# Performance work log

Measured on AMD Instinct MI355X. Metric: run time of the kernel, lower is better.

## Reference

```python
import jax, jax.numpy as jnp
import numpy as np

N, S, E, H = 4, 4096, 1024, 16
D = E // H  # 64


def setup_inputs() -> dict:
    key = jax.random.key(0)
    ks = jax.random.split(key, 6)
    scale = 0.02
    x = jax.random.normal(ks[0], (N, S, E), dtype=jnp.float32)
    Wq = jax.random.normal(ks[1], (E, E), dtype=jnp.float32) * scale
    Wk = jax.random.normal(ks[2], (E, E), dtype=jnp.float32) * scale
    Wv = jax.random.normal(ks[3], (E, E), dtype=jnp.float32) * scale
    Wo = jax.random.normal(ks[4], (E, E), dtype=jnp.float32) * scale
    bo = jax.random.normal(ks[5], (E,), dtype=jnp.float32) * scale
    return {"x": x, "Wq": Wq, "Wk": Wk, "Wv": Wv, "Wo": Wo, "bo": bo}


def reference(x, Wq, Wk, Wv, Wo, bo):
    n, s, _ = x.shape
    # torch nn.Linear(bias=False): y = x @ W.T  (W stored as [out, in])
    q = (x @ Wq.T).reshape(n, s, H, D).transpose(0, 2, 1, 3)  # (N, H, S, D)
    k = (x @ Wk.T).reshape(n, s, H, D).transpose(0, 2, 1, 3)  # (N, H, S, D)
    v = (x @ Wv.T).reshape(n, s, H, D).transpose(0, 2, 1, 3)  # (N, H, S, D)
    # Faithful to source: einsum subscripts applied to the PERMUTED (N,H,S,D)
    # tensors, so label q->H, h->S. energy: (N, H, H, S)
    energy = jnp.einsum('nqhd,nkhd->nqkh', q, k)
    attention = jax.nn.softmax(energy / (D ** 0.5), axis=3)
    # 'nqkh,nvhd->nqhd': k and v are independently summed free indices
    out = jnp.einsum('nqkh,nvhd->nqhd', attention, v).reshape(n, s, E)  # (N,S,E)
    return out @ Wo.T + bo
```

## Files before the change

### kernel.cpp

```cpp
#include <hip/hip_runtime.h>
#include <stdint.h>

typedef unsigned short u16;
typedef unsigned int   u32;
typedef __attribute__((ext_vector_type(8))) short short8;
typedef __attribute__((ext_vector_type(4))) float f32x4;
typedef __attribute__((ext_vector_type(8))) u16   u16x8;
typedef __attribute__((ext_vector_type(4))) u16   u16x4;

static constexpr size_t NX = (size_t)4 * 4096 * 1024;
static constexpr size_t NW = (size_t)1024 * 1024;

static constexpr size_t OFF_XB   = 0;
static constexpr size_t OFF_EN   = 0;
static constexpr size_t OFF_QK   = 33554432;
static constexpr size_t OFF_WQB  = 100663296;
static constexpr size_t OFF_WKB  = 102760448;
static constexpr size_t OFF_WOB  = 104857600;
static constexpr size_t OFF_WVST = 106954752;
static constexpr size_t OFF_VS   = 107216896;
static constexpr size_t OFF_GMAX = 111411200;
static constexpr size_t OFF_INVZ = 111415296;
static constexpr size_t OFF_ST   = 111419392;

static __device__ __forceinline__ u16 f2bf(float f) {
    u32 u = __builtin_bit_cast(u32, f);
    u += 0x7fffu + ((u >> 16) & 1u);
    return (u16)(u >> 16);
}
static __device__ __forceinline__ float bf2f(u16 v) {
    u32 u = ((u32)v) << 16;
    return __builtin_bit_cast(float, u);
}

#if __has_builtin(__builtin_amdgcn_global_load_lds)
#define HAVE_GLOAD_LDS 1
static __device__ __forceinline__ void gload_lds16(const void* g, void* l) {
    __builtin_amdgcn_global_load_lds(
        (__attribute__((address_space(1))) void*)(uintptr_t)g,
        (__attribute__((address_space(3))) void*)(uintptr_t)l,
        16, 0, 0);
}
#endif

#if __has_builtin(__builtin_amdgcn_sched_barrier)
#define SCHED_FENCE() __builtin_amdgcn_sched_barrier(0)
#else
#define SCHED_FENCE()
#endif

__global__ __launch_bounds__(256)
void cvt_all_kernel(const float* __restrict__ x, const float* __restrict__ wq,
                    const float* __restrict__ wk, const float* __restrict__ wv,
                    const float* __restrict__ wo,
                    u16* __restrict__ xb, u16* __restrict__ wqb,
                    u16* __restrict__ wkb, u16* __restrict__ wob,
                    u16* __restrict__ Bvs)
{
    const int blk = blockIdx.x;
    if (blk < 9728) {
        size_t i = ((size_t)blk * 256 + threadIdx.x) * 8;
        const float* s; u16* dst; size_t o;
        if (i < NX) { s = x; dst = xb; o = i; }
        else {
            size_t r = i - NX;
            int w = (int)(r >> 20);
            o = r & (NW - 1);
            s   = (w == 0) ? wq  : (w == 1) ? wk  : wo;
            dst = (w == 0) ? wqb : (w == 1) ? wkb : wob;
        }
        f32x4 a = *(const f32x4*)&s[o];
        f32x4 c = *(const f32x4*)&s[o + 4];
        u16x8 v;
        v[0]=f2bf(a[0]); v[1]=f2bf(a[1]); v[2]=f2bf(a[2]); v[3]=f2bf(a[3]);
        v[4]=f2bf(c[0]); v[5]=f2bf(c[1]); v[6]=f2bf(c[2]); v[7]=f2bf(c[3]);
        *(u16x8*)&dst[o] = v;
    } else {
        int idx = (blk - 9728) * 256 + threadIdx.x;
        int d = idx >> 10;
        int e = idx & 1023;
        float s = 0.f;
        #pragma unroll
        for (int h = 0; h < 16; ++h) s += wv[(size_t)(h * 64 + d) * 1024 + e];
        Bvs[(size_t)d * 1024 + e] = f2bf(s);
    }
}

__global__ __launch_bounds__(512, 2)
void gemm_qk(const u16* __restrict__ A, const u16* __restrict__ Bw,
             u16* __restrict__ C, int M, int N, int K, int lognbx)
{
    __shared__ u16 lds[65536];
    const int tid  = threadIdx.x;
    const int wave = tid >> 6;
    const int lane = tid & 63;

    const int nwg = gridDim.x;
    const int swz = ((int)blockIdx.x & 7) * (nwg >> 3) + ((int)blockIdx.x >> 3);
    const long col0 = (long)(swz & ((1 << lognbx) - 1)) * 256;
    const long row0 = (long)(swz >> lognbx) * 256;

    const int wr2 = wave >> 2;
    const int wc2 = wave & 3;
    const int fr  = lane & 15;
    const int kq  = lane >> 4;
    const int rxor = fr & 7;

    const int t255  = tid & 255;
    const int halfA = tid >> 8;
    const int gAsrc = (t255 & 7) ^ ((t255 >> 3) & 7);
    const u16* sA = A + (size_t)(row0 + halfA * 128 + (t255 >> 3)) * K + gAsrc * 8;
    const int dA = halfA * 8192 + t255 * 8;

    const int u  = (tid & 127) | ((tid >> 1) & 128);
    const int bh = (tid >> 7) & 1;
    const int gBsrc = (u & 7) ^ ((u >> 3) & 7);
    const u16* sB = Bw + (size_t)(col0 + bh * 128 + (u >> 3)) * K + gBsrc * 8;
    const int dB = bh * 8192 + u * 8;

    auto STAGE = [&](int buf, int k0) {
        #pragma unroll
        for (int l = 0; l < 4; ++l) {
#ifdef HAVE_GLOAD_LDS
            gload_lds16(sA + (size_t)l * 32 * K + k0, &lds[buf * 16384 + dA + l * 2048]);
            gload_lds16(sB + (size_t)l * 32 * K + k0, &lds[32768 + buf * 16384 + dB + l * 2048]);
#else
            *(short8*)&lds[buf * 16384 + dA + l * 2048] =
                *(const short8*)(sA + (size_t)l * 32 * K + k0);
            *(short8*)&lds[32768 + buf * 16384 + dB + l * 2048] =
                *(const short8*)(sB + (size_t)l * 32 * K + k0);
#endif
        }
    };

    f32x4 acc[8][4] = {};

    STAGE(0, 0);
    __syncthreads();

    const int nt = K >> 6;
    for (int t = 0; t < nt; ++t) {
        const int cur = t & 1;
        const int base  = cur * 16384;
        const int bbase = 32768 + cur * 16384;

        if (t + 1 < nt) STAGE(cur ^ 1, (t + 1) << 6);

        short8 af[4][2], ag[4][2], bf[2][2], bg[2][2];
        #pragma unroll
        for (int m = 0; m < 4; ++m) {
            const int row = wr2 * 128 + m * 16 + fr;
            #pragma unroll
            for (int kk = 0; kk < 2; ++kk)
                af[m][kk] = *(const short8*)&lds[base + row * 64 + (((kk << 2) | kq) ^ rxor) * 8];
        }
        #pragma unroll
        for (int n = 0; n < 2; ++n) {
            const int col = wc2 * 64 + n * 16 + fr;
            #pragma unroll
            for (int kk = 0; kk < 2; ++kk)
                bf[n][kk] = *(const short8*)&lds[bbase + col * 64 + (((kk << 2) | kq) ^ rxor) * 8];
        }
        #pragma unroll
        for (int m = 0; m < 4; ++m) {
            const int row = wr2 * 128 + 64 + m * 16 + fr;
            #pragma unroll
            for (int kk = 0; kk < 2; ++kk)
                ag[m][kk] = *(const short8*)&lds[base + row * 64 + (((kk << 2) | kq) ^ rxor) * 8];
        }
        SCHED_FENCE();

        __builtin_amdgcn_s_setprio(1);
        #pragma unroll
        for (int kk = 0; kk < 2; ++kk)
            #pragma unroll
            for (int m = 0; m < 4; ++m)
                #pragma unroll
                for (int n = 0; n < 2; ++n)
                    acc[m][n] = __builtin_amdgcn_mfma_f32_16x16x32_bf16(af[m][kk], bf[n][kk], acc[m][n], 0, 0, 0);
        __builtin_amdgcn_s_setprio(0);

        #pragma unroll
        for (int n = 0; n < 2; ++n) {
            const int col = wc2 * 64 + (n + 2) * 16 + fr;
            #pragma unroll
            for (int kk = 0; kk < 2; ++kk)
                bg[n][kk] = *(const short8*)&lds[bbase + col * 64 + (((kk << 2) | kq) ^ rxor) * 8];
        }
        SCHED_FENCE();

        __builtin_amdgcn_s_setprio(1);
        #pragma unroll
        for (int kk = 0; kk < 2; ++kk)
            #pragma unroll
            for (int m = 0; m < 4; ++m)
                #pragma unroll
                for (int n = 0; n < 2; ++n)
                    acc[m + 4][n] = __builtin_amdgcn_mfma_f32_16x16x32_bf16(ag[m][kk], bf[n][kk], acc[m + 4][n], 0, 0, 0);
        #pragma unroll
        for (int kk = 0; kk < 2; ++kk)
            #pragma unroll
            for (int m = 0; m < 4; ++m)
                #pragma unroll
                for (int n = 0; n < 2; ++n)
                    acc[m][n + 2] = __builtin_amdgcn_mfma_f32_16x16x32_bf16(af[m][kk], bg[n][kk], acc[m][n + 2], 0, 0, 0);
        #pragma unroll
        for (int kk = 0; kk < 2; ++kk)
            #pragma unroll
            for (int m = 0; m < 4; ++m)
                #pragma unroll
                for (int n = 0; n < 2; ++n)
                    acc[m + 4][n + 2] = __builtin_amdgcn_mfma_f32_16x16x32_bf16(ag[m][kk], bg[n][kk], acc[m + 4][n + 2], 0, 0, 0);
        __builtin_amdgcn_s_setprio(0);

        __syncthreads();
    }

    #pragma unroll
    for (int m = 0; m < 8; ++m) {
        #pragma unroll
        for (int n = 0; n < 4; ++n) {
            long gr = row0 + wr2 * 128 + m * 16 + kq * 4;
            long gc = col0 + wc2 * 64 + n * 16 + fr;
            #pragma unroll
            for (int j = 0; j < 4; ++j)
                C[(gr + j) * N + gc] = f2bf(acc[m][n][j]);
        }
    }
}

__global__ __launch_bounds__(256)
void gemm_vs(const u16* __restrict__ A, const u16* __restrict__ Bw,
             u16* __restrict__ C)
{
    __shared__ u16 lsA[2][64 * 32];
    __shared__ u16 lsB[2][64 * 32];
    const int tid  = threadIdx.x;
    const int wave = tid >> 6;
    const int lane = tid & 63;
    const long row0 = (long)blockIdx.x * 64;
    const int wr = (wave >> 1) * 32;
    const int wc = (wave & 1) * 32;
    const int fr = lane & 15;
    const int k8 = (lane >> 4) * 8;

    f32x4 acc[2][2] = {};
    const int c0 = tid;
    const u16* pa = &A [(row0 + (c0 >> 2)) * 1024 + (c0 & 3) * 8];
    const u16* pb = &Bw[((size_t)(c0 >> 2)) * 1024 + (c0 & 3) * 8];

    auto STAGE = [&](int buf, int k0) {
#ifdef HAVE_GLOAD_LDS
        gload_lds16(pa + k0, &lsA[buf][wave * 512]);
        gload_lds16(pb + k0, &lsB[buf][wave * 512]);
#else
        *(short8*)&lsA[buf][(size_t)c0 * 8] = *(const short8*)(pa + k0);
        *(short8*)&lsB[buf][(size_t)c0 * 8] = *(const short8*)(pb + k0);
#endif
    };

    STAGE(0, 0);
    __syncthreads();
    for (int t = 0; t < 32; ++t) {
        const int cur = t & 1;
        if (t + 1 < 32) STAGE(cur ^ 1, (t + 1) << 5);
        short8 af[2], bf[2];
        #pragma unroll
        for (int m = 0; m < 2; ++m)
            af[m] = *(const short8*)&lsA[cur][(wr + m * 16 + fr) * 32 + k8];
        #pragma unroll
        for (int n = 0; n < 2; ++n)
            bf[n] = *(const short8*)&lsB[cur][(wc + n * 16 + fr) * 32 + k8];
        #pragma unroll
        for (int m = 0; m < 2; ++m)
            #pragma unroll
            for (int n = 0; n < 2; ++n)
                acc[m][n] = __builtin_amdgcn_mfma_f32_16x16x32_bf16(af[m], bf[n], acc[m][n], 0, 0, 0);
        __syncthreads();
    }

    const int orow = (lane >> 4) * 4;
    #pragma unroll
    for (int m = 0; m < 2; ++m) {
        #pragma unroll
        for (int n = 0; n < 2; ++n) {
            long gr = row0 + wr + m * 16 + orow;
            int  gc = wc + n * 16 + fr;
            #pragma unroll
            for (int j = 0; j < 4; ++j)
                C[(gr + j) * 64 + gc] = f2bf(acc[m][n][j]);
        }
    }
}

__global__ __launch_bounds__(256)
void energy_stats_kernel(const u16* __restrict__ QKb, float* __restrict__ E,
                         float* __restrict__ pmax, float* __restrict__ psum)
{
    __shared__ float red[4][64][8];
    const int wave = threadIdx.x >> 6, lane = threadIdx.x & 63;
    const size_t s0 = (size_t)blockIdx.x * 64 + wave * 16;
    const int hh = lane & 15;
    const int kg = lane >> 4;
    float m[4] = {-3.4e38f, -3.4e38f, -3.4e38f, -3.4e38f};
    float z[4] = {0.f, 0.f, 0.f, 0.f};

    for (int s = 0; s < 16; ++s) {
        const u16* qrow = QKb + (s0 + s) * 2048;
        short8 a0 = *(const short8*)&qrow[hh * 64 + kg * 8];
        short8 a1 = *(const short8*)&qrow[hh * 64 + 32 + kg * 8];
        short8 b0 = *(const short8*)&qrow[1024 + hh * 64 + kg * 8];
        short8 b1 = *(const short8*)&qrow[1024 + hh * 64 + 32 + kg * 8];
        f32x4 acc = {};
        acc = __builtin_amdgcn_mfma_f32_16x16x32_bf16(a0, b0, acc, 0, 0, 0);
        acc = __builtin_amdgcn_mfma_f32_16x16x32_bf16(a1, b1, acc, 0, 0, 0);
        float* o = E + (s0 + s) * 256;
        #pragma unroll
        for (int r = 0; r < 4; ++r) {
            const float v = acc[r];
            o[(kg * 4 + r) * 16 + hh] = v;
            const float mn = fmaxf(m[r], v);
            z[r] = z[r] * __expf((m[r] - mn) * 0.125f) + __expf((v - mn) * 0.125f);
            m[r] = mn;
        }
    }
    #pragma unroll
    for (int r = 0; r < 4; ++r) { red[wave][lane][r] = m[r]; red[wave][lane][4 + r] = z[r]; }
    __syncthreads();

    const int t = threadIdx.x;
    const int i = t >> 4, j = t & 15;
    const int ln = (i >> 2) * 16 + j, r = i & 3;
    float M = -3.4e38f, Z = 0.f;
    #pragma unroll
    for (int w = 0; w < 4; ++w) {
        const float mw = red[w][ln][r], zw = red[w][ln][4 + r];
        const float mn = fmaxf(M, mw);
        Z = Z * __expf((M - mn) * 0.125f) + zw * __expf((mw - mn) * 0.125f);
        M = mn;
    }
    pmax[blockIdx.x * 256 + t] = M;
    psum[blockIdx.x * 256 + t] = Z;
}

__global__ __launch_bounds__(256)
void stats_comb(const float* __restrict__ pmax, const float* __restrict__ psum,
                float* __restrict__ gmax, float* __restrict__ invZ)
{
    const int n = blockIdx.x, p = threadIdx.x;
    float m = -3.4e38f;
    for (int c = 0; c < 64; ++c) m = fmaxf(m, pmax[(n * 64 + c) * 256 + p]);
    float z = 0.f;
    for (int c = 0; c < 64; ++c)
        z += psum[(n * 64 + c) * 256 + p] * __expf((pmax[(n * 64 + c) * 256 + p] - m) * 0.125f);
    gmax[n * 256 + p] = m;
    invZ[n * 256 + p] = 1.0f / z;
}

__global__ __launch_bounds__(256)
void g_kernel(const u16* __restrict__ Vsb, const u16* __restrict__ Wob,
              u16* __restrict__ G)
{
    __shared__ u16 lA[64 * 64];
    __shared__ u16 lB[256 * 64];
    const int tid = threadIdx.x;
    const int wave = tid >> 6, lane = tid & 63;
    const int op = blockIdx.x, uc = blockIdx.y, sl = blockIdx.z;

    {
        const int j = tid >> 2;
        const size_t srow = (size_t)16 * (64 * uc + j) + sl;
        #pragma unroll
        for (int h = 0; h < 2; ++h) {
            const int g = (tid & 3) + h * 4;
            u16x8 v = *(const u16x8*)&Vsb[srow * 64 + g * 8];
            *(u16x8*)&lA[j * 64 + ((g ^ (j & 7)) * 8)] = v;
        }
    }
    {
        const size_t o = (size_t)op * 256 + tid;
        #pragma unroll
        for (int g = 0; g < 8; ++g) {
            u16x8 v = *(const u16x8*)&Wob[o * 1024 + 64 * sl + g * 8];
            *(u16x8*)&lB[tid * 64 + ((g ^ (tid & 7)) * 8)] = v;
        }
    }
    __syncthreads();

    const int fr = lane & 15, kq = lane >> 4;
    f32x4 acc[4][4] = {};
    #pragma unroll
    for (int kk = 0; kk < 2; ++kk) {
        short8 af[4], bq[4];
        #pragma unroll
        for (int m = 0; m < 4; ++m) {
            const int j = m * 16 + fr;
            af[m] = *(const short8*)&lA[j * 64 + (((kq + 4 * kk) ^ (j & 7)) * 8)];
        }
        #pragma unroll
        for (int n = 0; n < 4; ++n) {
            const int o = wave * 64 + n * 16 + fr;
            bq[n] = *(const short8*)&lB[o * 64 + (((kq + 4 * kk) ^ (o & 7)) * 8)];
        }
        #pragma unroll
        for (int m = 0; m < 4; ++m)
            #pragma unroll
            for (int n = 0; n < 4; ++n)
                acc[m][n] = __builtin_amdgcn_mfma_f32_16x16x32_bf16(af[m], bq[n], acc[m][n], 0, 0, 0);
    }

    #pragma unroll
    for (int m = 0; m < 4; ++m) {
        #pragma unroll
        for (int n = 0; n < 4; ++n) {
            const int ocol = op * 256 + wave * 64 + n * 16 + fr;
            #pragma unroll
            for (int jj = 0; jj < 4; ++jj) {
                const int j = m * 16 + kq * 4 + jj;
                G[((size_t)16 * (64 * uc + j) + sl) * 1024 + ocol] = f2bf(acc[m][n][jj]);
            }
        }
    }
}

__global__ __launch_bounds__(256)
void comb_kernel(const float* __restrict__ En, const float* __restrict__ gmax,
                 const float* __restrict__ invZ, const u16* __restrict__ G,
                 const float* __restrict__ bo, float* __restrict__ out)
{
    __shared__ float sm[256], sz[256], sa[256];
    const int b = blockIdx.x;
    const int n = b >> 8, c = b & 255;
    const int t = threadIdx.x;
    sm[t] = gmax[n * 256 + t];
    sz[t] = invZ[n * 256 + t];
    __syncthreads();
    {
        const int sl = t >> 4, i = t & 15;
        const float* e = En + ((size_t)n * 4096 + c * 16 + sl) * 256 + i * 16;
        float a = 0.f;
        #pragma unroll
        for (int j = 0; j < 16; ++j)
            a += __expf((e[j] - sm[i * 16 + j]) * 0.125f) * sz[i * 16 + j];
        sa[sl * 16 + i] = a;
    }
    __syncthreads();

    const int o0 = t * 4;
    const u16* gp = G + ((size_t)n * 4096 + c * 16) * 1024 + o0;
    f32x4 g[16];
    #pragma unroll
    for (int sl = 0; sl < 16; ++sl) {
        u16x4 gv = *(const u16x4*)&gp[(size_t)sl * 1024];
        g[sl][0] = bf2f(gv[0]); g[sl][1] = bf2f(gv[1]);
        g[sl][2] = bf2f(gv[2]); g[sl][3] = bf2f(gv[3]);
    }
    const f32x4 b4 = *(const f32x4*)&bo[o0];
    #pragma unroll
    for (int i = 0; i < 16; ++i) {
        f32x4 acc = b4;
        #pragma unroll
        for (int sl = 0; sl < 16; ++sl) {
            const float a = sa[sl * 16 + i];
            acc[0] += a * g[sl][0];
            acc[1] += a * g[sl][1];
            acc[2] += a * g[sl][2];
            acc[3] += a * g[sl][3];
        }
        *(f32x4*)&out[((size_t)n * 4096 + i * 256 + c) * 1024 + o0] = acc;
    }
}

extern "C" void kernel_launch(void* const* d_in, const int* in_sizes, int n_in,
                              void* d_out, int out_size, void* d_ws, size_t ws_size,
                              hipStream_t stream)
{
    const float* x  = (const float*)d_in[0];
    const float* Wq = (const float*)d_in[1];
    const float* Wk = (const float*)d_in[2];
    const float* Wv = (const float*)d_in[3];
    const float* Wo = (const float*)d_in[4];
    const float* bo = (const float*)d_in[5];
    float* out = (float*)d_out;
    char* ws = (char*)d_ws;

    u16*   xb   = (u16*)  (ws + OFF_XB);
    float* En   = (float*)(ws + OFF_EN);
    u16*   QKb  = (u16*)  (ws + OFF_QK);
    u16*   G    = (u16*)  (ws + OFF_QK);
    u16*   Wqb  = (u16*)  (ws + OFF_WQB);
    u16*   Wkb  = (u16*)  (ws + OFF_WKB);
    u16*   Wob  = (u16*)  (ws + OFF_WOB);
    u16*   Bvs  = (u16*)  (ws + OFF_WVST);
    u16*   Vsb  = (u16*)  (ws + OFF_VS);
    float* gmax = (float*)(ws + OFF_GMAX);
    float* invZ = (float*)(ws + OFF_INVZ);
    float* pmax = (float*)(ws + OFF_ST);
    float* psum = (float*)(ws + OFF_ST + 262144);

    cvt_all_kernel<<<9984, 256, 0, stream>>>(x, Wq, Wk, Wv, Wo, xb, Wqb, Wkb, Wob, Bvs);

    gemm_qk<<<512, 512, 0, stream>>>(xb, Wqb, QKb, 16384, 2048, 1024, 3);
    gemm_vs<<<256, 256, 0, stream>>>(xb, Bvs, Vsb);

    energy_stats_kernel<<<256, 256, 0, stream>>>(QKb, En, pmax, psum);
    stats_comb<<<4, 256, 0, stream>>>(pmax, psum, gmax, invZ);

    g_kernel<<<dim3(4, 16, 16), 256, 0, stream>>>(Vsb, Wob, G);

    comb_kernel<<<1024, 256, 0, stream>>>(En, gmax, invZ, G, bo, out);
}
```

Baseline: 171.9 us.

## Widen gemm_vs to 512 threads with swizzled LDS and double energy-stats grid

gemm_vs now runs 8 waves per block. Half the threads stage A and half stage B, each wave computes a 16x32 tile, and LDS columns are XOR-swizzled to reduce bank conflicts. energy_stats_kernel processes 8 rows per wave over 512 blocks instead of 16 rows over 256, which doubles the partial stats buffer. stats_comb is unrolled with four independent accumulators over 128 partials. The aim is more parallelism and latency hiding on these small kernels, at the cost of more partial-reduction work and more blocks to schedule.

```diff
diff --git a/kernel.cpp b/kernel.cpp
--- a/kernel.cpp
+++ b/kernel.cpp
@@ -12,7 +12,6 @@
 static constexpr size_t NW = (size_t)1024 * 1024;
 
 static constexpr size_t OFF_XB   = 0;
-static constexpr size_t OFF_EN   = 0;
 static constexpr size_t OFF_QK   = 33554432;
 static constexpr size_t OFF_WQB  = 100663296;
 static constexpr size_t OFF_WKB  = 102760448;
@@ -229,7 +228,7 @@
     }
 }
 
-__global__ __launch_bounds__(256)
+__global__ __launch_bounds__(512)
 void gemm_vs(const u16* __restrict__ A, const u16* __restrict__ Bw,
              u16* __restrict__ C)
 {
@@ -239,23 +238,27 @@
     const int wave = tid >> 6;
     const int lane = tid & 63;
     const long row0 = (long)blockIdx.x * 64;
-    const int wr = (wave >> 1) * 32;
+    const int wr = (wave >> 1) * 16;
     const int wc = (wave & 1) * 32;
     const int fr = lane & 15;
-    const int k8 = (lane >> 4) * 8;
-
-    f32x4 acc[2][2] = {};
-    const int c0 = tid;
-    const u16* pa = &A [(row0 + (c0 >> 2)) * 1024 + (c0 & 3) * 8];
-    const u16* pb = &Bw[((size_t)(c0 >> 2)) * 1024 + (c0 & 3) * 8];
+    const int kq = lane >> 4;
+    const int rx = (fr >> 1) & 3;
+
+    f32x4 acc[2] = {};
+    const int g = tid & 255;
+    const int grow = g >> 2;
+    const int gsw  = (g & 3) ^ ((grow >> 1) & 3);
+    const bool isA = tid < 256;
+    const u16* src = isA ? &A [(row0 + grow) * 1024 + gsw * 8]
+                         : &Bw[((size_t)grow) * 1024 + gsw * 8];
 
     auto STAGE = [&](int buf, int k0) {
 #ifdef HAVE_GLOAD_LDS
-        gload_lds16(pa + k0, &lsA[buf][wave * 512]);
-        gload_lds16(pb + k0, &lsB[buf][wave * 512]);
+        if (isA) gload_lds16(src + k0, &lsA[buf][wave * 512]);
+        else     gload_lds16(src + k0, &lsB[buf][(wave - 4) * 512]);
 #else
-        *(short8*)&lsA[buf][(size_t)c0 * 8] = *(const short8*)(pa + k0);
-        *(short8*)&lsB[buf][(size_t)c0 * 8] = *(const short8*)(pb + k0);
+        if (isA) *(short8*)&lsA[buf][(size_t)g * 8] = *(const short8*)(src + k0);
+        else     *(short8*)&lsB[buf][(size_t)g * 8] = *(const short8*)(src + k0);
 #endif
     };
 
@@ -264,32 +267,23 @@
     for (int t = 0; t < 32; ++t) {
         const int cur = t & 1;
         if (t + 1 < 32) STAGE(cur ^ 1, (t + 1) << 5);
-        short8 af[2], bf[2];
-        #pragma unroll
-        for (int m = 0; m < 2; ++m)
-            af[m] = *(const short8*)&lsA[cur][(wr + m * 16 + fr) * 32 + k8];
+        short8 af, bf[2];
+        af = *(const short8*)&lsA[cur][(wr + fr) * 32 + ((kq ^ rx) * 8)];
         #pragma unroll
         for (int n = 0; n < 2; ++n)
-            bf[n] = *(const short8*)&lsB[cur][(wc + n * 16 + fr) * 32 + k8];
-        #pragma unroll
-        for (int m = 0; m < 2; ++m)
-            #pragma unroll
-            for (int n = 0; n < 2; ++n)
-                acc[m][n] = __builtin_amdgcn_mfma_f32_16x16x32_bf16(af[m], bf[n], acc[m][n], 0, 0, 0);
+            bf[n] = *(const short8*)&lsB[cur][(wc + n * 16 + fr) * 32 + ((kq ^ rx) * 8)];
+        #pragma unroll
+        for (int n = 0; n < 2; ++n)
+            acc[n] = __builtin_amdgcn_mfma_f32_16x16x32_bf16(af, bf[n], acc[n], 0, 0, 0);
         __syncthreads();
     }
 
-    const int orow = (lane >> 4) * 4;
-    #pragma unroll
-    for (int m = 0; m < 2; ++m) {
-        #pragma unroll
-        for (int n = 0; n < 2; ++n) {
-            long gr = row0 + wr + m * 16 + orow;
-            int  gc = wc + n * 16 + fr;
-            #pragma unroll
-            for (int j = 0; j < 4; ++j)
-                C[(gr + j) * 64 + gc] = f2bf(acc[m][n][j]);
-        }
+    const int orow = kq * 4;
+    #pragma unroll
+    for (int n = 0; n < 2; ++n) {
+        #pragma unroll
+        for (int j = 0; j < 4; ++j)
+            C[(row0 + wr + orow + j) * 64 + wc + n * 16 + fr] = f2bf(acc[n][j]);
     }
 }
 
@@ -299,13 +293,13 @@
 {
     __shared__ float red[4][64][8];
     const int wave = threadIdx.x >> 6, lane = threadIdx.x & 63;
-    const size_t s0 = (size_t)blockIdx.x * 64 + wave * 16;
+    const size_t s0 = (size_t)blockIdx.x * 32 + wave * 8;
     const int hh = lane & 15;
     const int kg = lane >> 4;
     float m[4] = {-3.4e38f, -3.4e38f, -3.4e38f, -3.4e38f};
     float z[4] = {0.f, 0.f, 0.f, 0.f};
 
-    for (int s = 0; s < 16; ++s) {
+    for (int s = 0; s < 8; ++s) {
         const u16* qrow = QKb + (s0 + s) * 2048;
         short8 a0 = *(const short8*)&qrow[hh * 64 + kg * 8];
         short8 a1 = *(const short8*)&qrow[hh * 64 + 32 + kg * 8];
@@ -348,13 +342,24 @@
                 float* __restrict__ gmax, float* __restrict__ invZ)
 {
     const int n = blockIdx.x, p = threadIdx.x;
-    float m = -3.4e38f;
-    for (int c = 0; c < 64; ++c) m = fmaxf(m, pmax[(n * 64 + c) * 256 + p]);
-    float z = 0.f;
-    for (int c = 0; c < 64; ++c)
-        z += psum[(n * 64 + c) * 256 + p] * __expf((pmax[(n * 64 + c) * 256 + p] - m) * 0.125f);
-    gmax[n * 256 + p] = m;
-    invZ[n * 256 + p] = 1.0f / z;
+    const float* pm = pmax + (size_t)n * 128 * 256 + p;
+    const float* ps = psum + (size_t)n * 128 * 256 + p;
+    float m[4] = {-3.4e38f, -3.4e38f, -3.4e38f, -3.4e38f};
+    for (int c = 0; c < 32; ++c) {
+        #pragma unroll
+        for (int u = 0; u < 4; ++u)
+            m[u] = fmaxf(m[u], pm[(size_t)(c + u * 32) * 256]);
+    }
+    const float M = fmaxf(fmaxf(m[0], m[1]), fmaxf(m[2], m[3]));
+    float z[4] = {0.f, 0.f, 0.f, 0.f};
+    for (int c = 0; c < 32; ++c) {
+        #pragma unroll
+        for (int u = 0; u < 4; ++u)
+            z[u] += ps[(size_t)(c + u * 32) * 256] *
+                    __expf((pm[(size_t)(c + u * 32) * 256] - M) * 0.125f);
+    }
+    gmax[n * 256 + p] = M;
+    invZ[n * 256 + p] = 1.0f / (z[0] + z[1] + z[2] + z[3]);
 }
 
 __global__ __launch_bounds__(256)
@@ -485,7 +490,7 @@
     char* ws = (char*)d_ws;
 
     u16*   xb   = (u16*)  (ws + OFF_XB);
-    float* En   = (float*)(ws + OFF_EN);
+    float* En   = (float*)(ws + OFF_XB);
     u16*   QKb  = (u16*)  (ws + OFF_QK);
     u16*   G    = (u16*)  (ws + OFF_QK);
     u16*   Wqb  = (u16*)  (ws + OFF_WQB);
@@ -496,14 +501,14 @@
     float* gmax = (float*)(ws + OFF_GMAX);
     float* invZ = (float*)(ws + OFF_INVZ);
     float* pmax = (float*)(ws + OFF_ST);
-    float* psum = (float*)(ws + OFF_ST + 262144);
+    float* psum = (float*)(ws + OFF_ST + 524288);
 
     cvt_all_kernel<<<9984, 256, 0, stream>>>(x, Wq, Wk, Wv, Wo, xb, Wqb, Wkb, Wob, Bvs);
 
     gemm_qk<<<512, 512, 0, stream>>>(xb, Wqb, QKb, 16384, 2048, 1024, 3);
-    gemm_vs<<<256, 256, 0, stream>>>(xb, Bvs, Vsb);
-
-    energy_stats_kernel<<<256, 256, 0, stream>>>(QKb, En, pmax, psum);
+    gemm_vs<<<256, 512, 0, stream>>>(xb, Bvs, Vsb);
+
+    energy_stats_kernel<<<512, 256, 0, stream>>>(QKb, En, pmax, psum);
     stats_comb<<<4, 256, 0, stream>>>(pmax, psum, gmax, invZ);
 
     g_kernel<<<dim3(4, 16, 16), 256, 0, stream>>>(Vsb, Wob, G);
```

Result: faster. 162.9 us (-5.3%).
